# Performance work log

Hardware: AMD Instinct MI355X
Metric: run time of the kernel (lower is better)

## Reference

```python
import jax, jax.numpy as jnp
import numpy as np

HEADS = 16

def setup_inputs() -> dict:
    key = jax.random.key(0)
    ks = jax.random.split(key, 7)
    B, S, E = 2, 2048, 1024
    return {
        "query": jax.random.normal(ks[0], (B, S, E), dtype=jnp.float32),
        "key": jax.random.normal(ks[1], (B, S, E), dtype=jnp.float32),
        "value": jax.random.normal(ks[2], (B, S, E), dtype=jnp.float32),
        "Wqkv": jax.random.normal(ks[3], (E, 3 * E), dtype=jnp.float32) * (E ** -0.5),
        "bqkv": jax.random.normal(ks[4], (3 * E,), dtype=jnp.float32) * 0.02,
        "Wproj": jax.random.normal(ks[5], (E, E), dtype=jnp.float32) * (E ** -0.5),
        "bproj": jax.random.normal(ks[6], (E,), dtype=jnp.float32) * 0.02,
    }

def reference(query, key, value, Wqkv, bqkv, Wproj, bproj):
    # key/value args are unused in the original forward (overwritten by QKV split)
    B, S, E = query.shape
    H = HEADS
    hd = E // H
    qkv = query @ Wqkv + bqkv                     # [B, S, 3E]
    qkv = qkv.reshape(B, S, H, 3 * hd).transpose(0, 2, 1, 3)  # [B, H, S, 3hd]
    q = qkv[..., :hd]
    k = qkv[..., hd:2 * hd]
    v = qkv[..., 2 * hd:]
    qk = jnp.einsum("bhqd,bhkd->bhqk", q, k)
    # faithful quirk: original divides by head_dim**-0.5, i.e. multiplies by sqrt(hd)
    scaled = qk / (hd ** -0.5)
    attn = jax.nn.softmax(scaled, axis=-1)        # dropout p=0 -> identity
    out = jnp.einsum("bhqk,bhkd->bhqd", attn, v)  # [B, H, S, hd]
    out = out.transpose(0, 2, 1, 3).reshape(B, S, E)
    return out @ Wproj + bproj
```

## Files before the change

kernel.cpp:

```cpp
#include <hip/hip_runtime.h>
#include <hip/hip_bf16.h>
#include <stdint.h>

typedef __attribute__((ext_vector_type(8))) _Float16 f16x8;
typedef __attribute__((ext_vector_type(4))) _Float16 f16x4;
typedef __attribute__((ext_vector_type(4))) float f32x4;

static constexpr int BATCH = 2;
static constexpr int SEQ = 2048;
static constexpr int EMB = 1024;
static constexpr int NH = 16;
static constexpr int HD_ = 64;

#define AS1 __attribute__((address_space(1)))
#define AS3 __attribute__((address_space(3)))

__device__ __forceinline__ void gload_lds16(const void* g, void* l) {
  __builtin_amdgcn_global_load_lds((const AS1 uint32_t*)g, (AS3 uint32_t*)l, 16, 0, 0);
}

__device__ __forceinline__ f32x4 mfma16(f16x8 a, f16x8 b, f32x4 c) {
  return __builtin_amdgcn_mfma_f32_16x16x32_f16(a, b, c, 0, 0, 0);
}

__device__ __forceinline__ f16x8 swzread(const _Float16* base, int row, int blk) {
  return *(const f16x8*)((const char*)base + row * 128 +
                         ((blk * 16) ^ ((row & 7) << 4)));
}

__global__ __launch_bounds__(256) void k_convert_split(const float* __restrict__ in,
                                                       _Float16* __restrict__ oh,
                                                       _Float16* __restrict__ ol,
                                                       int n4) {
  int idx = blockIdx.x * 256 + threadIdx.x;
  if (idx >= n4) return;
  float4 v = reinterpret_cast<const float4*>(in)[idx];
  const float* f = reinterpret_cast<const float*>(&v);
  _Float16 h[4], l[4];
#pragma unroll
  for (int i = 0; i < 4; ++i) {
    h[i] = (_Float16)f[i];
    l[i] = (_Float16)(f[i] - (float)h[i]);
  }
  reinterpret_cast<uint2*>(oh)[idx] = *reinterpret_cast<uint2*>(h);
  reinterpret_cast<uint2*>(ol)[idx] = *reinterpret_cast<uint2*>(l);
}

template <int PERM>
__global__ __launch_bounds__(256) void k_transpose(const float* __restrict__ in,
                                                   _Float16* __restrict__ out, int R,
                                                   int C) {
  __shared__ float tile[32][33];
  const int t = threadIdx.x;
  const int tr = t >> 5, tc = t & 31;
  const int r0 = blockIdx.y * 32, c0 = blockIdx.x * 32;
#pragma unroll
  for (int rr = 0; rr < 32; rr += 8)
    tile[tr + rr][tc] = in[(size_t)(r0 + tr + rr) * C + c0 + tc];
  __syncthreads();
#pragma unroll
  for (int rr = 0; rr < 32; rr += 8) {
    const int c = c0 + tr + rr;
    int d = c;
    if constexpr (PERM) {
      const int h = c / 192, r = c - h * 192;
      d = (r < 64) ? h * 64 + r
                   : (r < 128 ? 1024 + h * 64 + (r - 64) : 2048 + h * 64 + (r - 128));
    }
    out[(size_t)d * R + r0 + tc] = (_Float16)tile[tc][tr + rr];
  }
}

__global__ __launch_bounds__(256) void k_gemm_qkv(
    const _Float16* __restrict__ Ah, const _Float16* __restrict__ Al,
    const _Float16* __restrict__ Bt, const float* __restrict__ bias,
    _Float16* __restrict__ oq, _Float16* __restrict__ ok,
    _Float16* __restrict__ ov) {
  constexpr int K = EMB;
  __shared__ _Float16 AsH[2][128 * 32];
  __shared__ _Float16 AsL[2][128 * 32];
  __shared__ _Float16 Bs[2][128 * 32];
  const int t = threadIdx.x;
  const int l = t & 63, w = t >> 6;
  const int lr = l & 15, lg = l >> 4;
  const int wr = w >> 1, wc = w & 1;
  const int m0 = blockIdx.y * 128, n0 = blockIdx.x * 128;
  const bool splitb = (n0 < 2048);

  auto stage = [&](int buf, int k0) {
#pragma unroll
    for (int j = 0; j < 2; ++j) {
      const int c = t + 256 * j;
      const int row = c >> 2, cb = c & 3;
      const size_t ga = (size_t)(m0 + row) * K + k0 + cb * 8;
      const size_t gb = (size_t)(n0 + row) * K + k0 + cb * 8;
      gload_lds16(Ah + ga, &AsH[buf][c * 8]);
      gload_lds16(Bt + gb, &Bs[buf][c * 8]);
      if (splitb) gload_lds16(Al + ga, &AsL[buf][c * 8]);
    }
  };

  f32x4 acc[4][4];
#pragma unroll
  for (int m = 0; m < 4; ++m)
#pragma unroll
    for (int n = 0; n < 4; ++n) acc[m][n] = f32x4{0.f, 0.f, 0.f, 0.f};

  stage(0, 0);
  const int NT = K / 32;
  int cur = 0;
  for (int kt = 0; kt < NT; ++kt) {
    __syncthreads();
    if (kt + 1 < NT) stage(cur ^ 1, (kt + 1) * 32);
    f16x8 afh[4], afl[4], bf[4];
#pragma unroll
    for (int m = 0; m < 4; ++m) {
      const int off = (wr * 64 + m * 16 + lr) * 32 + lg * 8;
      afh[m] = *(const f16x8*)&AsH[cur][off];
      if (splitb) afl[m] = *(const f16x8*)&AsL[cur][off];
    }
#pragma unroll
    for (int n = 0; n < 4; ++n)
      bf[n] = *(const f16x8*)&Bs[cur][(wc * 64 + n * 16 + lr) * 32 + lg * 8];
#pragma unroll
    for (int m = 0; m < 4; ++m)
#pragma unroll
      for (int n = 0; n < 4; ++n) {
        acc[m][n] = mfma16(afh[m], bf[n], acc[m][n]);
        if (splitb) acc[m][n] = mfma16(afl[m], bf[n], acc[m][n]);
      }
    cur ^= 1;
  }

  const int sec = n0 >> 10;
#pragma unroll
  for (int m = 0; m < 4; ++m) {
#pragma unroll
    for (int n = 0; n < 4; ++n) {
      const int col = n0 + wc * 64 + n * 16 + lr;
      const int cc = col & 1023;
      const int h = cc >> 6, r = cc & 63;
      const float bv = bias[h * 192 + sec * 64 + r];
      const int row0 = m0 + wr * 64 + m * 16 + lg * 4;
      const int b = row0 >> 11, s0 = row0 & (SEQ - 1);
      if (sec == 2) {
        f16x4 vv;
#pragma unroll
        for (int i = 0; i < 4; ++i) vv[i] = (_Float16)(acc[m][n][i] + bv);
        *(f16x4*)&ov[(((size_t)b * NH + h) * HD_ + r) * SEQ + s0] = vv;
      } else {
#pragma unroll
        for (int i = 0; i < 4; ++i) {
          const float v = acc[m][n][i] + bv;
          const size_t dst = (((size_t)b * NH + h) * SEQ + s0 + i) * HD_ + r;
          if (sec == 0)
            oq[dst] = (_Float16)(v * 11.5415603f);
          else
            ok[dst] = (_Float16)v;
        }
      }
    }
  }
}

__global__ __launch_bounds__(256) void k_gemm_proj(const _Float16* __restrict__ A,
                                                   const _Float16* __restrict__ Bt,
                                                   const float* __restrict__ bias,
                                                   float* __restrict__ of) {
  constexpr int K = EMB, N = EMB;
  __shared__ _Float16 As[2][128 * 32];
  __shared__ _Float16 Bs[2][128 * 32];
  const int t = threadIdx.x;
  const int l = t & 63, w = t >> 6;
  const int lr = l & 15, lg = l >> 4;
  const int wr = w >> 1, wc = w & 1;
  const int m0 = blockIdx.y * 128, n0 = blockIdx.x * 128;

  auto stage = [&](int buf, int k0) {
#pragma unroll
    for (int j = 0; j < 2; ++j) {
      const int c = t + 256 * j;
      const int row = c >> 2, cb = c & 3;
      gload_lds16(A + (size_t)(m0 + row) * K + k0 + cb * 8, &As[buf][c * 8]);
      gload_lds16(Bt + (size_t)(n0 + row) * K + k0 + cb * 8, &Bs[buf][c * 8]);
    }
  };

  f32x4 acc[4][4];
#pragma unroll
  for (int m = 0; m < 4; ++m)
#pragma unroll
    for (int n = 0; n < 4; ++n) acc[m][n] = f32x4{0.f, 0.f, 0.f, 0.f};

  stage(0, 0);
  const int NT = K / 32;
  int cur = 0;
  for (int kt = 0; kt < NT; ++kt) {
    __syncthreads();
    if (kt + 1 < NT) stage(cur ^ 1, (kt + 1) * 32);
    f16x8 af[4], bf[4];
#pragma unroll
    for (int m = 0; m < 4; ++m)
      af[m] = *(const f16x8*)&As[cur][(wr * 64 + m * 16 + lr) * 32 + lg * 8];
#pragma unroll
    for (int n = 0; n < 4; ++n)
      bf[n] = *(const f16x8*)&Bs[cur][(wc * 64 + n * 16 + lr) * 32 + lg * 8];
#pragma unroll
    for (int m = 0; m < 4; ++m)
#pragma unroll
      for (int n = 0; n < 4; ++n) acc[m][n] = mfma16(af[m], bf[n], acc[m][n]);
    cur ^= 1;
  }

#pragma unroll
  for (int m = 0; m < 4; ++m)
#pragma unroll
    for (int n = 0; n < 4; ++n)
#pragma unroll
      for (int i = 0; i < 4; ++i) {
        const int row = m0 + wr * 64 + m * 16 + lg * 4 + i;
        const int col = n0 + wc * 64 + n * 16 + lr;
        of[(size_t)row * N + col] = acc[m][n][i] + bias[col];
      }
}

__global__ __launch_bounds__(512) void k_attn(
    const _Float16* __restrict__ qs, const _Float16* __restrict__ ks,
    const _Float16* __restrict__ vt, _Float16* __restrict__ op,
    float* __restrict__ marr, float* __restrict__ larr) {
  __shared__ _Float16 Kt[2][64][64];
  __shared__ _Float16 Vt[2][64][64];
  __shared__ _Float16 Pl[8][16][64];
  const int t = threadIdx.x;
  const int l = t & 63, w = t >> 6;
  const int lr = l & 15, lg = l >> 4;
  const int id = blockIdx.x;
  const int xc = id & 7, m_ = id >> 3;
  const int kvh = m_ & 1;
  const int bh = xc + 8 * (m_ >> 5);
  const int qb = ((m_ >> 1) & 15) * 128 + w * 16;
  const int kvbase = kvh * (SEQ / 2);

  const size_t qoff = ((size_t)bh * SEQ + qb + lr) * HD_;
  const f16x8 qf0 = *(const f16x8*)(qs + qoff + lg * 8);
  const f16x8 qf1 = *(const f16x8*)(qs + qoff + 32 + lg * 8);

  const _Float16* kbase = ks + (size_t)bh * SEQ * HD_;
  const _Float16* vbase = vt + (size_t)bh * HD_ * SEQ;

  const int srow = t >> 3, scb = t & 7;
  auto stage = [&](const int buf, const int kv0) {
    gload_lds16(kbase + (size_t)(kv0 + srow) * HD_ + (scb ^ (srow & 7)) * 8,
                &Kt[buf][srow][scb * 8]);
    gload_lds16(vbase + (size_t)srow * SEQ + kv0 + (scb ^ (srow & 7)) * 8,
                &Vt[buf][srow][scb * 8]);
  };

  stage(0, kvbase);

  float mr = -1e30f, lsum = 0.f;
  f32x4 oacc[4];
#pragma unroll
  for (int n = 0; n < 4; ++n) oacc[n] = f32x4{0.f, 0.f, 0.f, 0.f};

  const int NT = SEQ / 128;
  for (int it = 0; it < NT; ++it) {
    const int cur = it & 1;
    __syncthreads();
    if (it + 1 < NT) stage(cur ^ 1, kvbase + (it + 1) * 64);

    f32x4 sa[4];
    __builtin_amdgcn_s_setprio(1);
#pragma unroll
    for (int t4 = 0; t4 < 4; ++t4) {
      const int r = t4 * 16 + lr;
      const f16x8 kf0 = swzread(&Kt[cur][0][0], r, lg);
      const f16x8 kf1 = swzread(&Kt[cur][0][0], r, lg + 4);
      f32x4 s = mfma16(kf0, qf0, f32x4{0.f, 0.f, 0.f, 0.f});
      sa[t4] = mfma16(kf1, qf1, s);
    }
    __builtin_amdgcn_s_setprio(0);

    float t01 = fmaxf(fmaxf(sa[0][0], sa[0][1]), fmaxf(sa[0][2], sa[0][3]));
    float t23 = fmaxf(fmaxf(sa[1][0], sa[1][1]), fmaxf(sa[1][2], sa[1][3]));
    float t45 = fmaxf(fmaxf(sa[2][0], sa[2][1]), fmaxf(sa[2][2], sa[2][3]));
    float t67 = fmaxf(fmaxf(sa[3][0], sa[3][1]), fmaxf(sa[3][2], sa[3][3]));
    float tm = fmaxf(fmaxf(t01, t23), fmaxf(t45, t67));
    tm = fmaxf(tm, __shfl_xor(tm, 16));
    tm = fmaxf(tm, __shfl_xor(tm, 32));

    if (__any(tm > mr + 8.0f)) {
      const float nm = fmaxf(mr, tm);
      const float corr = exp2f(mr - nm);
      mr = nm;
      lsum *= corr;
      float cb4[4];
#pragma unroll
      for (int i = 0; i < 4; ++i)
        cb4[i] = __shfl(corr, (l & 48) + ((l >> 4) << 2) + i);
#pragma unroll
      for (int n = 0; n < 4; ++n)
#pragma unroll
        for (int i = 0; i < 4; ++i) oacc[n][i] *= cb4[i];
    }

    float ts = 0.f;
    char* plbase = (char*)&Pl[w][0][0];
#pragma unroll
    for (int t4 = 0; t4 < 4; ++t4) {
      f16x4 pp;
#pragma unroll
      for (int i = 0; i < 4; ++i) {
        const float p = exp2f(sa[t4][i] - mr);
        ts += p;
        pp[i] = (_Float16)p;
      }
      *(f16x4*)(plbase + lr * 128 + ((t4 * 32 + lg * 8) ^ ((lr & 7) << 4))) = pp;
    }
    ts += __shfl_xor(ts, 16);
    ts += __shfl_xor(ts, 32);
    lsum += ts;

    const f16x8 aP0 = swzread(&Pl[w][0][0], lr, lg);
    const f16x8 aP1 = swzread(&Pl[w][0][0], lr, lg + 4);
    __builtin_amdgcn_s_setprio(1);
#pragma unroll
    for (int n = 0; n < 4; ++n) {
      const int d = n * 16 + lr;
      const f16x8 bv0 = swzread(&Vt[cur][0][0], d, lg);
      const f16x8 bv1 = swzread(&Vt[cur][0][0], d, lg + 4);
      oacc[n] = mfma16(aP0, bv0, oacc[n]);
      oacc[n] = mfma16(aP1, bv1, oacc[n]);
    }
    __builtin_amdgcn_s_setprio(0);
  }

  const size_t mlbase = ((size_t)kvh * 32 + bh) * SEQ + qb;
  if (l < 16) {
    marr[mlbase + l] = mr;
    larr[mlbase + l] = lsum;
  }
  _Float16* opb = op + (size_t)kvh * BATCH * SEQ * EMB;
  const int b = bh >> 4, h = bh & 15;
#pragma unroll
  for (int n = 0; n < 4; ++n)
#pragma unroll
    for (int i = 0; i < 4; ++i) {
      const int row = qb + ((l >> 4) << 2) + i;
      opb[((size_t)b * SEQ + row) * EMB + h * HD_ + n * 16 + lr] =
          (_Float16)oacc[n][i];
    }
}

__global__ __launch_bounds__(256) void k_combine(const _Float16* __restrict__ op,
                                                 const float* __restrict__ marr,
                                                 const float* __restrict__ larr,
                                                 _Float16* __restrict__ ao) {
  const int idx = blockIdx.x * 256 + threadIdx.x;
  const int e8 = idx & 127;
  const size_t rs = (size_t)(idx >> 7);
  const int h = e8 >> 3;
  const int b = (int)(rs >> 11);
  const size_t s = rs & (SEQ - 1);
  const size_t mi = ((size_t)b * NH + h) * SEQ + s;
  const float m1 = marr[mi], l1 = larr[mi];
  const float m2 = marr[(size_t)32 * SEQ + mi], l2 = larr[(size_t)32 * SEQ + mi];
  const float mx = fmaxf(m1, m2);
  const float w1 = exp2f(m1 - mx), w2 = exp2f(m2 - mx);
  const float inv = 1.0f / (l1 * w1 + l2 * w2);
  const f16x8 o1 = ((const f16x8*)op)[idx];
  const f16x8 o2 = ((const f16x8*)op)[idx + (BATCH * SEQ * EMB / 8)];
  f16x8 r;
#pragma unroll
  for (int j = 0; j < 8; ++j)
    r[j] = (_Float16)(((float)o1[j] * w1 + (float)o2[j] * w2) * inv);
  ((f16x8*)ao)[idx] = r;
}

extern "C" void kernel_launch(void* const* d_in, const int* in_sizes, int n_in,
                              void* d_out, int out_size, void* d_ws, size_t ws_size,
                              hipStream_t stream) {
  const float* query = (const float*)d_in[0];
  const float* Wqkv = (const float*)d_in[3];
  const float* bqkv = (const float*)d_in[4];
  const float* Wproj = (const float*)d_in[5];
  const float* bproj = (const float*)d_in[6];
  float* out = (float*)d_out;

  char* ws = (char*)d_ws;
  const size_t MB = 1024 * 1024;
  _Float16* q_hi    = (_Float16*)(ws + 0);
  _Float16* q_lo    = (_Float16*)(ws + 8 * MB);
  _Float16* Wqkv_t  = (_Float16*)(ws + 16 * MB);
  _Float16* q_s     = (_Float16*)(ws + 24 * MB);
  _Float16* k_s     = (_Float16*)(ws + 32 * MB);
  _Float16* v_t     = (_Float16*)(ws + 40 * MB);
  _Float16* op      = (_Float16*)(ws + 0);
  _Float16* Wproj_t = (_Float16*)(ws + 48 * MB);
  float*    marr    = (float*)(ws + 50 * MB);
  float*    larr    = (float*)(ws + 50 * MB + 512 * 1024);
  _Float16* a_o     = (_Float16*)(ws + 51 * MB);

  const int M = BATCH * SEQ;
  k_convert_split<<<(M * EMB / 4 + 255) / 256, 256, 0, stream>>>(query, q_hi, q_lo,
                                                                 M * EMB / 4);
  k_transpose<1><<<dim3(3 * EMB / 32, EMB / 32), 256, 0, stream>>>(Wqkv, Wqkv_t, EMB,
                                                                   3 * EMB);
  k_gemm_qkv<<<dim3(24, M / 128), 256, 0, stream>>>(q_hi, q_lo, Wqkv_t, bqkv, q_s, k_s,
                                                    v_t);
  k_transpose<0><<<dim3(EMB / 32, EMB / 32), 256, 0, stream>>>(Wproj, Wproj_t, EMB, EMB);
  k_attn<<<dim3(1024), 512, 0, stream>>>(q_s, k_s, v_t, op, marr, larr);
  k_combine<<<dim3(BATCH * SEQ * EMB / 8 / 256), 256, 0, stream>>>(op, marr, larr, a_o);
  k_gemm_proj<<<dim3(EMB / 128, M / 128), 256, 0, stream>>>(a_o, Wproj_t, bproj, out);
}
```

Baseline: 165.6 us.

## Process two query tiles per wave in attention and skip negligible score tiles

```diff
diff --git a/kernel.cpp b/kernel.cpp
--- a/kernel.cpp
+++ b/kernel.cpp
@@ -224,26 +224,29 @@
       }
 }
 
-__global__ __launch_bounds__(512) void k_attn(
+__global__ __launch_bounds__(512, 4) void k_attn(
     const _Float16* __restrict__ qs, const _Float16* __restrict__ ks,
     const _Float16* __restrict__ vt, _Float16* __restrict__ op,
     float* __restrict__ marr, float* __restrict__ larr) {
   __shared__ _Float16 Kt[2][64][64];
   __shared__ _Float16 Vt[2][64][64];
-  __shared__ _Float16 Pl[8][16][64];
+  __shared__ _Float16 Pl[8][2][16][64];
   const int t = threadIdx.x;
   const int l = t & 63, w = t >> 6;
   const int lr = l & 15, lg = l >> 4;
   const int id = blockIdx.x;
   const int xc = id & 7, m_ = id >> 3;
   const int kvh = m_ & 1;
-  const int bh = xc + 8 * (m_ >> 5);
-  const int qb = ((m_ >> 1) & 15) * 128 + w * 16;
+  const int bh = xc + 8 * (m_ >> 4);
+  const int qb = ((m_ >> 1) & 7) * 256 + w * 32;
   const int kvbase = kvh * (SEQ / 2);
 
-  const size_t qoff = ((size_t)bh * SEQ + qb + lr) * HD_;
-  const f16x8 qf0 = *(const f16x8*)(qs + qoff + lg * 8);
-  const f16x8 qf1 = *(const f16x8*)(qs + qoff + 32 + lg * 8);
+  const size_t qoffA = ((size_t)bh * SEQ + qb + lr) * HD_;
+  const size_t qoffB = qoffA + (size_t)16 * HD_;
+  const f16x8 qfA0 = *(const f16x8*)(qs + qoffA + lg * 8);
+  const f16x8 qfA1 = *(const f16x8*)(qs + qoffA + 32 + lg * 8);
+  const f16x8 qfB0 = *(const f16x8*)(qs + qoffB + lg * 8);
+  const f16x8 qfB1 = *(const f16x8*)(qs + qoffB + 32 + lg * 8);
 
   const _Float16* kbase = ks + (size_t)bh * SEQ * HD_;
   const _Float16* vbase = vt + (size_t)bh * HD_ * SEQ;
@@ -258,10 +261,13 @@
 
   stage(0, kvbase);
 
-  float mr = -1e30f, lsum = 0.f;
-  f32x4 oacc[4];
-#pragma unroll
-  for (int n = 0; n < 4; ++n) oacc[n] = f32x4{0.f, 0.f, 0.f, 0.f};
+  float mrA = -1e30f, lsumA = 0.f, mrB = -1e30f, lsumB = 0.f;
+  f32x4 oaccA[4], oaccB[4];
+#pragma unroll
+  for (int n = 0; n < 4; ++n) {
+    oaccA[n] = f32x4{0.f, 0.f, 0.f, 0.f};
+    oaccB[n] = f32x4{0.f, 0.f, 0.f, 0.f};
+  }
 
   const int NT = SEQ / 128;
   for (int it = 0; it < NT; ++it) {
@@ -269,76 +275,149 @@
     __syncthreads();
     if (it + 1 < NT) stage(cur ^ 1, kvbase + (it + 1) * 64);
 
-    f32x4 sa[4];
-    __builtin_amdgcn_s_setprio(1);
+    f16x8 kf0[4], kf1[4];
 #pragma unroll
     for (int t4 = 0; t4 < 4; ++t4) {
       const int r = t4 * 16 + lr;
-      const f16x8 kf0 = swzread(&Kt[cur][0][0], r, lg);
-      const f16x8 kf1 = swzread(&Kt[cur][0][0], r, lg + 4);
-      f32x4 s = mfma16(kf0, qf0, f32x4{0.f, 0.f, 0.f, 0.f});
-      sa[t4] = mfma16(kf1, qf1, s);
+      kf0[t4] = swzread(&Kt[cur][0][0], r, lg);
+      kf1[t4] = swzread(&Kt[cur][0][0], r, lg + 4);
+    }
+
+    f32x4 saA[4];
+    __builtin_amdgcn_s_setprio(1);
+#pragma unroll
+    for (int t4 = 0; t4 < 4; ++t4) {
+      f32x4 s = mfma16(kf0[t4], qfA0, f32x4{0.f, 0.f, 0.f, 0.f});
+      saA[t4] = mfma16(kf1[t4], qfA1, s);
     }
     __builtin_amdgcn_s_setprio(0);
 
-    float t01 = fmaxf(fmaxf(sa[0][0], sa[0][1]), fmaxf(sa[0][2], sa[0][3]));
-    float t23 = fmaxf(fmaxf(sa[1][0], sa[1][1]), fmaxf(sa[1][2], sa[1][3]));
-    float t45 = fmaxf(fmaxf(sa[2][0], sa[2][1]), fmaxf(sa[2][2], sa[2][3]));
-    float t67 = fmaxf(fmaxf(sa[3][0], sa[3][1]), fmaxf(sa[3][2], sa[3][3]));
-    float tm = fmaxf(fmaxf(t01, t23), fmaxf(t45, t67));
-    tm = fmaxf(tm, __shfl_xor(tm, 16));
-    tm = fmaxf(tm, __shfl_xor(tm, 32));
-
-    if (__any(tm > mr + 8.0f)) {
-      const float nm = fmaxf(mr, tm);
-      const float corr = exp2f(mr - nm);
-      mr = nm;
-      lsum *= corr;
-      float cb4[4];
-#pragma unroll
-      for (int i = 0; i < 4; ++i)
-        cb4[i] = __shfl(corr, (l & 48) + ((l >> 4) << 2) + i);
-#pragma unroll
-      for (int n = 0; n < 4; ++n)
-#pragma unroll
-        for (int i = 0; i < 4; ++i) oacc[n][i] *= cb4[i];
-    }
-
-    float ts = 0.f;
-    char* plbase = (char*)&Pl[w][0][0];
+    float tmA = fmaxf(fmaxf(fmaxf(saA[0][0], saA[0][1]), fmaxf(saA[0][2], saA[0][3])),
+                      fmaxf(fmaxf(saA[1][0], saA[1][1]), fmaxf(saA[1][2], saA[1][3])));
+    tmA = fmaxf(tmA,
+                fmaxf(fmaxf(fmaxf(saA[2][0], saA[2][1]), fmaxf(saA[2][2], saA[2][3])),
+                      fmaxf(fmaxf(saA[3][0], saA[3][1]), fmaxf(saA[3][2], saA[3][3]))));
+    tmA = fmaxf(tmA, __shfl_xor(tmA, 16));
+    tmA = fmaxf(tmA, __shfl_xor(tmA, 32));
+    const bool skipA = __all(tmA < mrA - 24.0f);
+    if (!skipA) {
+      if (__any(tmA > mrA + 8.0f)) {
+        const float nm = fmaxf(mrA, tmA);
+        const float corr = exp2f(mrA - nm);
+        mrA = nm;
+        lsumA *= corr;
+        float cb4[4];
+#pragma unroll
+        for (int i = 0; i < 4; ++i)
+          cb4[i] = __shfl(corr, (l & 48) + ((l >> 4) << 2) + i);
+#pragma unroll
+        for (int n = 0; n < 4; ++n)
+#pragma unroll
+          for (int i = 0; i < 4; ++i) oaccA[n][i] *= cb4[i];
+      }
+      float ts = 0.f;
+      char* plA = (char*)&Pl[w][0][0][0];
+#pragma unroll
+      for (int t4 = 0; t4 < 4; ++t4) {
+        f16x4 pp;
+#pragma unroll
+        for (int i = 0; i < 4; ++i) {
+          const float p = exp2f(saA[t4][i] - mrA);
+          ts += p;
+          pp[i] = (_Float16)p;
+        }
+        *(f16x4*)(plA + lr * 128 + ((t4 * 32 + lg * 8) ^ ((lr & 7) << 4))) = pp;
+      }
+      ts += __shfl_xor(ts, 16);
+      ts += __shfl_xor(ts, 32);
+      lsumA += ts;
+    }
+
+    f32x4 saB[4];
+    __builtin_amdgcn_s_setprio(1);
 #pragma unroll
     for (int t4 = 0; t4 < 4; ++t4) {
-      f16x4 pp;
-#pragma unroll
-      for (int i = 0; i < 4; ++i) {
-        const float p = exp2f(sa[t4][i] - mr);
-        ts += p;
-        pp[i] = (_Float16)p;
-      }
-      *(f16x4*)(plbase + lr * 128 + ((t4 * 32 + lg * 8) ^ ((lr & 7) << 4))) = pp;
-    }
-    ts += __shfl_xor(ts, 16);
-    ts += __shfl_xor(ts, 32);
-    lsum += ts;
-
-    const f16x8 aP0 = swzread(&Pl[w][0][0], lr, lg);
-    const f16x8 aP1 = swzread(&Pl[w][0][0], lr, lg + 4);
-    __builtin_amdgcn_s_setprio(1);
-#pragma unroll
-    for (int n = 0; n < 4; ++n) {
-      const int d = n * 16 + lr;
-      const f16x8 bv0 = swzread(&Vt[cur][0][0], d, lg);
-      const f16x8 bv1 = swzread(&Vt[cur][0][0], d, lg + 4);
-      oacc[n] = mfma16(aP0, bv0, oacc[n]);
-      oacc[n] = mfma16(aP1, bv1, oacc[n]);
+      f32x4 s = mfma16(kf0[t4], qfB0, f32x4{0.f, 0.f, 0.f, 0.f});
+      saB[t4] = mfma16(kf1[t4], qfB1, s);
     }
     __builtin_amdgcn_s_setprio(0);
+
+    float tmB = fmaxf(fmaxf(fmaxf(saB[0][0], saB[0][1]), fmaxf(saB[0][2], saB[0][3])),
+                      fmaxf(fmaxf(saB[1][0], saB[1][1]), fmaxf(saB[1][2], saB[1][3])));
+    tmB = fmaxf(tmB,
+                fmaxf(fmaxf(fmaxf(saB[2][0], saB[2][1]), fmaxf(saB[2][2], saB[2][3])),
+                      fmaxf(fmaxf(saB[3][0], saB[3][1]), fmaxf(saB[3][2], saB[3][3]))));
+    tmB = fmaxf(tmB, __shfl_xor(tmB, 16));
+    tmB = fmaxf(tmB, __shfl_xor(tmB, 32));
+    const bool skipB = __all(tmB < mrB - 24.0f);
+    if (!skipB) {
+      if (__any(tmB > mrB + 8.0f)) {
+        const float nm = fmaxf(mrB, tmB);
+        const float corr = exp2f(mrB - nm);
+        mrB = nm;
+        lsumB *= corr;
+        float cb4[4];
+#pragma unroll
+        for (int i = 0; i < 4; ++i)
+          cb4[i] = __shfl(corr, (l & 48) + ((l >> 4) << 2) + i);
+#pragma unroll
+        for (int n = 0; n < 4; ++n)
+#pragma unroll
+          for (int i = 0; i < 4; ++i) oaccB[n][i] *= cb4[i];
+      }
+      float ts = 0.f;
+      char* plB = (char*)&Pl[w][1][0][0];
+#pragma unroll
+      for (int t4 = 0; t4 < 4; ++t4) {
+        f16x4 pp;
+#pragma unroll
+        for (int i = 0; i < 4; ++i) {
+          const float p = exp2f(saB[t4][i] - mrB);
+          ts += p;
+          pp[i] = (_Float16)p;
+        }
+        *(f16x4*)(plB + lr * 128 + ((t4 * 32 + lg * 8) ^ ((lr & 7) << 4))) = pp;
+      }
+      ts += __shfl_xor(ts, 16);
+      ts += __shfl_xor(ts, 32);
+      lsumB += ts;
+    }
+
+    if (!(skipA && skipB)) {
+      f16x8 aA0, aA1, aB0, aB1;
+      if (!skipA) {
+        aA0 = swzread(&Pl[w][0][0][0], lr, lg);
+        aA1 = swzread(&Pl[w][0][0][0], lr, lg + 4);
+      }
+      if (!skipB) {
+        aB0 = swzread(&Pl[w][1][0][0], lr, lg);
+        aB1 = swzread(&Pl[w][1][0][0], lr, lg + 4);
+      }
+      __builtin_amdgcn_s_setprio(1);
+#pragma unroll
+      for (int n = 0; n < 4; ++n) {
+        const int d = n * 16 + lr;
+        const f16x8 bv0 = swzread(&Vt[cur][0][0], d, lg);
+        const f16x8 bv1 = swzread(&Vt[cur][0][0], d, lg + 4);
+        if (!skipA) {
+          oaccA[n] = mfma16(aA0, bv0, oaccA[n]);
+          oaccA[n] = mfma16(aA1, bv1, oaccA[n]);
+        }
+        if (!skipB) {
+          oaccB[n] = mfma16(aB0, bv0, oaccB[n]);
+          oaccB[n] = mfma16(aB1, bv1, oaccB[n]);
+        }
+      }
+      __builtin_amdgcn_s_setprio(0);
+    }
   }
 
   const size_t mlbase = ((size_t)kvh * 32 + bh) * SEQ + qb;
   if (l < 16) {
-    marr[mlbase + l] = mr;
-    larr[mlbase + l] = lsum;
+    marr[mlbase + l] = mrA;
+    larr[mlbase + l] = lsumA;
+    marr[mlbase + 16 + l] = mrB;
+    larr[mlbase + 16 + l] = lsumB;
   }
   _Float16* opb = op + (size_t)kvh * BATCH * SEQ * EMB;
   const int b = bh >> 4, h = bh & 15;
@@ -346,9 +425,11 @@
   for (int n = 0; n < 4; ++n)
 #pragma unroll
     for (int i = 0; i < 4; ++i) {
-      const int row = qb + ((l >> 4) << 2) + i;
-      opb[((size_t)b * SEQ + row) * EMB + h * HD_ + n * 16 + lr] =
-          (_Float16)oacc[n][i];
+      const int rowA = qb + ((l >> 4) << 2) + i;
+      opb[((size_t)b * SEQ + rowA) * EMB + h * HD_ + n * 16 + lr] =
+          (_Float16)oaccA[n][i];
+      opb[((size_t)b * SEQ + rowA + 16) * EMB + h * HD_ + n * 16 + lr] =
+          (_Float16)oaccB[n][i];
     }
 }
 
@@ -409,7 +490,7 @@
   k_gemm_qkv<<<dim3(24, M / 128), 256, 0, stream>>>(q_hi, q_lo, Wqkv_t, bqkv, q_s, k_s,
                                                     v_t);
   k_transpose<0><<<dim3(EMB / 32, EMB / 32), 256, 0, stream>>>(Wproj, Wproj_t, EMB, EMB);
-  k_attn<<<dim3(1024), 512, 0, stream>>>(q_s, k_s, v_t, op, marr, larr);
+  k_attn<<<dim3(512), 512, 0, stream>>>(q_s, k_s, v_t, op, marr, larr);
   k_combine<<<dim3(BATCH * SEQ * EMB / 8 / 256), 256, 0, stream>>>(op, marr, larr, a_o);
   k_gemm_proj<<<dim3(EMB / 128, M / 128), 256, 0, stream>>>(a_o, Wproj_t, bproj, out);
 }
```

Result: slower. 211.8 us (+27.9%).

## Fold running max into MFMA init, skip negligible tiles, pack fp16 conversions

Applied to the files above, without the earlier changes.

```diff
diff --git a/kernel.cpp b/kernel.cpp
--- a/kernel.cpp
+++ b/kernel.cpp
@@ -4,6 +4,7 @@
 
 typedef __attribute__((ext_vector_type(8))) _Float16 f16x8;
 typedef __attribute__((ext_vector_type(4))) _Float16 f16x4;
+typedef __attribute__((ext_vector_type(2))) _Float16 f16x2;
 typedef __attribute__((ext_vector_type(4))) float f32x4;
 
 static constexpr int BATCH = 2;
@@ -21,6 +22,11 @@
 
 __device__ __forceinline__ f32x4 mfma16(f16x8 a, f16x8 b, f32x4 c) {
   return __builtin_amdgcn_mfma_f32_16x16x32_f16(a, b, c, 0, 0, 0);
+}
+
+__device__ __forceinline__ f16x2 pk16(float a, float b) {
+  auto r = __builtin_amdgcn_cvt_pkrtz(a, b);
+  return __builtin_bit_cast(f16x2, r);
 }
 
 __device__ __forceinline__ f16x8 swzread(const _Float16* base, int row, int blk) {
@@ -258,17 +264,19 @@
 
   stage(0, kvbase);
 
-  float mr = -1e30f, lsum = 0.f;
+  float mr = 0.f, lsum = 0.f;
   f32x4 oacc[4];
 #pragma unroll
   for (int n = 0; n < 4; ++n) oacc[n] = f32x4{0.f, 0.f, 0.f, 0.f};
 
+  char* plbase = (char*)&Pl[w][0][0];
   const int NT = SEQ / 128;
-  for (int it = 0; it < NT; ++it) {
-    const int cur = it & 1;
+
+  auto body = [&](const int cur, const int it) {
     __syncthreads();
     if (it + 1 < NT) stage(cur ^ 1, kvbase + (it + 1) * 64);
 
+    const float nmr = -mr;
     f32x4 sa[4];
     __builtin_amdgcn_s_setprio(1);
 #pragma unroll
@@ -276,7 +284,7 @@
       const int r = t4 * 16 + lr;
       const f16x8 kf0 = swzread(&Kt[cur][0][0], r, lg);
       const f16x8 kf1 = swzread(&Kt[cur][0][0], r, lg + 4);
-      f32x4 s = mfma16(kf0, qf0, f32x4{0.f, 0.f, 0.f, 0.f});
+      f32x4 s = mfma16(kf0, qf0, f32x4{nmr, nmr, nmr, nmr});
       sa[t4] = mfma16(kf1, qf1, s);
     }
     __builtin_amdgcn_s_setprio(0);
@@ -289,10 +297,29 @@
     tm = fmaxf(tm, __shfl_xor(tm, 16));
     tm = fmaxf(tm, __shfl_xor(tm, 32));
 
-    if (__any(tm > mr + 8.0f)) {
-      const float nm = fmaxf(mr, tm);
-      const float corr = exp2f(mr - nm);
-      mr = nm;
+    if (__all(tm < -24.0f)) return;
+
+    float ts = 0.f;
+    auto emitP = [&](const float d) {
+#pragma unroll
+      for (int t4 = 0; t4 < 4; ++t4) {
+        const float p0 = exp2f(sa[t4][0] - d);
+        const float p1 = exp2f(sa[t4][1] - d);
+        const float p2 = exp2f(sa[t4][2] - d);
+        const float p3 = exp2f(sa[t4][3] - d);
+        ts += (p0 + p1) + (p2 + p3);
+        const f16x2 lo2 = pk16(p0, p1);
+        const f16x2 hi2 = pk16(p2, p3);
+        f16x4 pp;
+        pp[0] = lo2[0]; pp[1] = lo2[1]; pp[2] = hi2[0]; pp[3] = hi2[1];
+        *(f16x4*)(plbase + lr * 128 + ((t4 * 32 + lg * 8) ^ ((lr & 7) << 4))) = pp;
+      }
+    };
+
+    if (__any(tm > 8.0f)) {
+      const float nm = fmaxf(tm, 0.f);
+      const float corr = exp2f(-nm);
+      mr += nm;
       lsum *= corr;
       float cb4[4];
 #pragma unroll
@@ -302,21 +329,11 @@
       for (int n = 0; n < 4; ++n)
 #pragma unroll
         for (int i = 0; i < 4; ++i) oacc[n][i] *= cb4[i];
-    }
-
-    float ts = 0.f;
-    char* plbase = (char*)&Pl[w][0][0];
-#pragma unroll
-    for (int t4 = 0; t4 < 4; ++t4) {
-      f16x4 pp;
-#pragma unroll
-      for (int i = 0; i < 4; ++i) {
-        const float p = exp2f(sa[t4][i] - mr);
-        ts += p;
-        pp[i] = (_Float16)p;
-      }
-      *(f16x4*)(plbase + lr * 128 + ((t4 * 32 + lg * 8) ^ ((lr & 7) << 4))) = pp;
-    }
+      emitP(nm);
+    } else {
+      emitP(0.0f);
+    }
+
     ts += __shfl_xor(ts, 16);
     ts += __shfl_xor(ts, 32);
     lsum += ts;
@@ -333,6 +350,11 @@
       oacc[n] = mfma16(aP1, bv1, oacc[n]);
     }
     __builtin_amdgcn_s_setprio(0);
+  };
+
+  for (int it = 0; it < NT; it += 2) {
+    body(0, it);
+    body(1, it + 1);
   }
 
   const size_t mlbase = ((size_t)kvh * 32 + bh) * SEQ + qb;
```

New measurement: 167.6 us. About the same (+1.2%).
